# Performance work log

Hardware: AMD Instinct MI355X
Metric: run time of the kernel (lower is better)

Reference implementation:

```python
import jax, jax.numpy as jnp
import numpy as np

HIDDEN_DIM = 64
VOCAB_SIZE = 64
MEMORY_SLOTS = 8
SEQ_LEN = 32
B = 32768


def setup_inputs() -> dict:
    key = jax.random.key(0)
    ks = jax.random.split(key, 11)
    s = 0.1
    return {
        "seqs": jax.random.randint(ks[0], (B, SEQ_LEN), 0, VOCAB_SIZE),
        "query_tok": jax.random.randint(ks[1], (B,), 0, VOCAB_SIZE),
        "embed_table": jax.random.normal(ks[2], (VOCAB_SIZE + 2, HIDDEN_DIM), jnp.float32) * s,
        "sc_w1": jax.random.normal(ks[3], (HIDDEN_DIM, 32), jnp.float32) * s,
        "sc_b1": jax.random.normal(ks[4], (32,), jnp.float32) * s,
        "sc_w2": jax.random.normal(ks[5], (32, 1), jnp.float32) * s,
        "sc_b2": jax.random.normal(ks[6], (1,), jnp.float32) * s,
        "rh_w1": jax.random.normal(ks[7], (2 * HIDDEN_DIM, HIDDEN_DIM), jnp.float32) * s,
        "rh_b1": jax.random.normal(ks[8], (HIDDEN_DIM,), jnp.float32) * s,
        "rh_w2": jax.random.normal(ks[9], (HIDDEN_DIM, VOCAB_SIZE), jnp.float32) * s,
        "rh_b2": jax.random.normal(ks[10], (VOCAB_SIZE,), jnp.float32) * s,
    }


def reference(seqs, query_tok, embed_table, sc_w1, sc_b1, sc_w2, sc_b2,
              rh_w1, rh_b1, rh_w2, rh_b2):
    # Embed the first SEQ_LEN-1 tokens: [B, 31, H]
    embs = embed_table[seqs[:, : SEQ_LEN - 1]]
    slot_ids = jnp.arange(MEMORY_SLOTS)

    def scan_one(embs_b):
        def step(carry, emb):
            mem, count = carry  # mem: [8, H], count: scalar int32
            # score all slots (harmless during fill phase; only used when full)
            scores = (jnp.maximum(mem @ sc_w1 + sc_b1, 0.0) @ sc_w2 + sc_b2)[:, 0]
            evict_idx = jnp.argmin(scores)
            # full: pop evict_idx (shift left above it), append new emb at slot 7
            rolled = jnp.roll(mem, -1, axis=0)
            full_mem = jnp.where(slot_ids[:, None] < evict_idx, mem, rolled)
            full_mem = full_mem.at[MEMORY_SLOTS - 1].set(emb)
            # filling: write new emb at position `count`
            fill_mem = mem.at[jnp.clip(count, 0, MEMORY_SLOTS - 1)].set(emb)
            new_mem = jnp.where(count >= MEMORY_SLOTS, full_mem, fill_mem)
            new_count = jnp.minimum(count + 1, MEMORY_SLOTS)
            return (new_mem, new_count), None

        init = (jnp.zeros((MEMORY_SLOTS, HIDDEN_DIM), embs_b.dtype),
                jnp.array(0, jnp.int32))
        (mem, _), _ = jax.lax.scan(step, init, embs_b)
        return mem.mean(0)  # memory is always full (31 tokens > 8 slots)

    mem_summary = jax.vmap(scan_one)(embs)  # [B, H]
    q_emb = embed_table[query_tok]          # [B, H]
    h = jnp.concatenate([q_emb, mem_summary], axis=-1)  # [B, 2H]
    return jnp.maximum(h @ rh_w1 + rh_b1, 0.0) @ rh_w2 + rh_b2  # [B, VOCAB]
```

## Files before the change

kernel.cpp:

```cpp
#include <hip/hip_runtime.h>


#define SEQ_LEN 32
#define MEM_SLOTS 8

#define WS_SCORE 0
#define WS_Q1B   64
#define WS_M2P   (64 + 4096)
#define WS_W2B   (64 + 4096 + 2048)

typedef __attribute__((ext_vector_type(8)))  short short8;
typedef __attribute__((ext_vector_type(16))) float floatx16;

__device__ __forceinline__ uint32_t bf16rtne(float f) {
    uint32_t u = __float_as_uint(f);
    return (u + 0x7FFFu + ((u >> 16) & 1u)) >> 16;
}

__global__ __launch_bounds__(256) void lem_precompute(
    const float* __restrict__ embed,
    const float* __restrict__ sc_w1, const float* __restrict__ sc_b1,
    const float* __restrict__ sc_w2, const float* __restrict__ sc_b2,
    const float* __restrict__ rh_w1, const float* __restrict__ rh_b1,
    const float* __restrict__ rh_w2,
    float* __restrict__ ws)
{
    const int t = threadIdx.x;
    const int blk = blockIdx.x;
    if (blk < 16) {
        const int p = blk * 256 + t;
        const int v = p >> 6, k = p & 63;
        const float* e = embed + v * 64;
        float q = rh_b1[k];
        #pragma unroll 8
        for (int i = 0; i < 64; ++i) q = fmaf(e[i], rh_w1[i * 64 + k], q);
        ws[WS_Q1B + v * 64 + k] = q;
    } else if (blk < 24) {
        const int p = (blk - 16) * 256 + t;
        const int v = p >> 5, j = p & 31;
        const float* e = embed + v * 64;
        float m0 = 0.f, m1 = 0.f;
        #pragma unroll 8
        for (int i = 0; i < 64; ++i) {
            const float ei = e[i];
            m0 = fmaf(ei, rh_w1[(64 + i) * 64 + 2 * j + 0], m0);
            m1 = fmaf(ei, rh_w1[(64 + i) * 64 + 2 * j + 1], m1);
        }
        ((uint32_t*)ws)[WS_M2P + j * 64 + v] =
            bf16rtne(m0 * 0.125f) | (bf16rtne(m1 * 0.125f) << 16);
    } else {
        __shared__ float part[2048];
        #pragma unroll
        for (int r = 0; r < 8; ++r) {
            const int s = r * 256 + t;
            const int v = s >> 5, k = s & 31;
            const float* e = embed + v * 64;
            float a = sc_b1[k];
            #pragma unroll 8
            for (int i = 0; i < 64; ++i) a = fmaf(e[i], sc_w1[i * 32 + k], a);
            a = fmaxf(a, 0.f);
            part[s] = a * sc_w2[k];
        }
        uint32_t* wb = (uint32_t*)ws + WS_W2B;
        #pragma unroll
        for (int r = 0; r < 8; ++r) {
            const int sidx = r * 256 + t;
            const int d = sidx & 3;
            const int ln = (sidx >> 2) & 63;
            const int tile = sidx >> 8;
            const int ktile = tile >> 1, tn = tile & 1;
            const int k = ktile * 16 + (ln >> 5) * 8 + 2 * d;
            const int n = tn * 32 + (ln & 31);
            wb[sidx] = bf16rtne(rh_w2[k * 64 + n]) |
                       (bf16rtne(rh_w2[(k + 1) * 64 + n]) << 16);
        }
        __syncthreads();
        if (t < 64) {
            float s = sc_b2[0];
            for (int k = 0; k < 32; ++k) s += part[t * 32 + k];
            ws[WS_SCORE + t] = s;
        }
    }
}

__global__ __launch_bounds__(256) void lem_main(
    const int* __restrict__ seqs, const int* __restrict__ qtok,
    const float* __restrict__ rh_b2,
    const float* __restrict__ ws, float* __restrict__ out)
{
    __shared__ uint32_t MT2[2048];
    __shared__ float score_s[64];
    __shared__ unsigned long long tok_s[64];
    __shared__ uint32_t hh2[2048];

    const int t = threadIdx.x;
    const int gbase = blockIdx.x * 64;
    const int lane = t & 63;
    const int w = t >> 6;
    const int col = t & 31;
    const int half = (t >> 5) & 1;
    const int tile_n = w & 1;
    const int tile_m = w >> 1;

    uint4 bq[4];
    const uint4* B4 = (const uint4*)((const uint32_t*)ws + WS_W2B);
    #pragma unroll
    for (int kt = 0; kt < 4; ++kt)
        bq[kt] = B4[(kt * 2 + tile_n) * 64 + lane];
    const float bias = rh_b2[tile_n * 32 + col];
    const int qb = qtok[gbase + lane];
    float4 qreg[4];
    {
        const float4* Q4 = (const float4*)(ws + WS_Q1B);
        const int qbase = (qb * 64 + w * 16) >> 2;
        #pragma unroll
        for (int j4 = 0; j4 < 4; ++j4) qreg[j4] = Q4[qbase + j4];
    }

    if (w == 0) {
        score_s[lane] = ws[WS_SCORE + lane];
        const int b = gbase + lane;
        int tk[SEQ_LEN];
        const int4* sq4 = (const int4*)(seqs + (long long)b * SEQ_LEN);
        #pragma unroll
        for (int r = 0; r < SEQ_LEN / 4; ++r) {
            int4 v = sq4[r];
            tk[r * 4 + 0] = v.x; tk[r * 4 + 1] = v.y;
            tk[r * 4 + 2] = v.z; tk[r * 4 + 3] = v.w;
        }
        int tok[MEM_SLOTS]; float sc[MEM_SLOTS];
        #pragma unroll
        for (int j = 0; j < MEM_SLOTS; ++j) tok[j] = tk[j];
        #pragma unroll
        for (int j = 0; j < MEM_SLOTS; ++j) sc[j] = score_s[tok[j]];
        #pragma unroll
        for (int step = MEM_SLOTS; step < SEQ_LEN - 1; ++step) {
            const int nt = tk[step];
            const float ns = score_s[nt];
            float bv = sc[0]; int be = 0;
            #pragma unroll
            for (int j = 1; j < MEM_SLOTS; ++j) {
                const bool lt = sc[j] < bv;
                bv = lt ? sc[j] : bv;
                be = lt ? j : be;
            }
            #pragma unroll
            for (int j = 0; j < MEM_SLOTS - 1; ++j) {
                const bool take = (j >= be);
                sc[j]  = take ? sc[j + 1]  : sc[j];
                tok[j] = take ? tok[j + 1] : tok[j];
            }
            sc[MEM_SLOTS - 1] = ns;
            tok[MEM_SLOTS - 1] = nt;
        }
        unsigned long long pk = 0ull;
        #pragma unroll
        for (int j = 0; j < MEM_SLOTS; ++j)
            pk |= (unsigned long long)(tok[j] & 255) << (8 * j);
        tok_s[lane] = pk;
    } else {
        const uint4* src = (const uint4*)((const uint32_t*)ws + WS_M2P);
        uint4* dst = (uint4*)MT2;
        for (int i = t - 64; i < 512; i += 192) dst[i] = src[i];
    }
    __syncthreads();

    const int b = lane;
    const unsigned long long pk = tok_s[b];

    float acc[16];
    #pragma unroll
    for (int j4 = 0; j4 < 4; ++j4) {
        acc[j4 * 4 + 0] = qreg[j4].x; acc[j4 * 4 + 1] = qreg[j4].y;
        acc[j4 * 4 + 2] = qreg[j4].z; acc[j4 * 4 + 3] = qreg[j4].w;
    }
    #pragma unroll
    for (int j = 0; j < MEM_SLOTS; ++j) {
        const int tkn = (int)((pk >> (8 * j)) & 255);
        #pragma unroll
        for (int jj = 0; jj < 8; ++jj) {
            const uint32_t u = MT2[(w * 8 + jj) * 64 + tkn];
            acc[2 * jj + 0] += __uint_as_float(u << 16);
            acc[2 * jj + 1] += __uint_as_float(u & 0xFFFF0000u);
        }
    }
    #pragma unroll
    for (int jj = 0; jj < 8; ++jj) {
        const uint32_t lo = (__float_as_uint(fmaxf(acc[2 * jj + 0], 0.f)) + 0x8000u) >> 16;
        const uint32_t hi = (__float_as_uint(fmaxf(acc[2 * jj + 1], 0.f)) + 0x8000u) >> 16;
        hh2[(w * 8 + jj) * 64 + b] = lo | (hi << 16);
    }
    __syncthreads();

    floatx16 oacc;
    #pragma unroll
    for (int i = 0; i < 16; ++i) oacc[i] = bias;

    union U8 { uint32_t u[4]; short8 s; };
    #pragma unroll
    for (int kt = 0; kt < 4; ++kt) {
        U8 a;
        #pragma unroll
        for (int d = 0; d < 4; ++d)
            a.u[d] = hh2[(kt * 8 + half * 4 + d) * 64 + (tile_m * 32 + col)];
        U8 bb;
        bb.u[0] = bq[kt].x; bb.u[1] = bq[kt].y;
        bb.u[2] = bq[kt].z; bb.u[3] = bq[kt].w;
        oacc = __builtin_amdgcn_mfma_f32_32x32x16_bf16(a.s, bb.s, oacc, 0, 0, 0);
    }

    #pragma unroll
    for (int reg = 0; reg < 16; ++reg) {
        const int row = (reg & 3) + 8 * (reg >> 2) + 4 * half;
        out[(long long)(gbase + tile_m * 32 + row) * 64 + tile_n * 32 + col] = oacc[reg];
    }
}

extern "C" void kernel_launch(void* const* d_in, const int* in_sizes, int n_in,
                              void* d_out, int out_size, void* d_ws, size_t ws_size,
                              hipStream_t stream)
{
    const int*   seqs   = (const int*)d_in[0];
    const int*   qtok   = (const int*)d_in[1];
    const float* embed  = (const float*)d_in[2];
    const float* sc_w1  = (const float*)d_in[3];
    const float* sc_b1  = (const float*)d_in[4];
    const float* sc_w2  = (const float*)d_in[5];
    const float* sc_b2  = (const float*)d_in[6];
    const float* rh_w1  = (const float*)d_in[7];
    const float* rh_b1  = (const float*)d_in[8];
    const float* rh_w2  = (const float*)d_in[9];
    const float* rh_b2  = (const float*)d_in[10];
    float* out = (float*)d_out;
    float* ws  = (float*)d_ws;

    const int B = in_sizes[1];

    lem_precompute<<<25, 256, 0, stream>>>(embed, sc_w1, sc_b1, sc_w2, sc_b2,
                                           rh_w1, rh_b1, rh_w2, ws);
    lem_main<<<B / 64, 256, 0, stream>>>(seqs, qtok, rh_b2, ws, out);
}
```

Before: 93.08 us.

## Double block to 512 threads and switch output GEMM to 16x16x32 MFMA tiles

Each block now uses 8 waves instead of 4, so every wave gathers and sums only 8 hidden columns instead of 16. The output GEMM switches from 32x32x16 to 16x16x32 bf16 MFMA, with each wave computing two 16x16 tiles, and the rh_w2 packing in precompute is reordered to match. The hidden buffer in shared memory is padded to a stride of 66 to reduce bank conflicts. The serial eviction scan is still run by one wave per block, so the extra waves mostly sit idle at the barrier.

```diff
diff --git a/kernel.cpp b/kernel.cpp
--- a/kernel.cpp
+++ b/kernel.cpp
@@ -9,8 +9,10 @@
 #define WS_M2P   (64 + 4096)
 #define WS_W2B   (64 + 4096 + 2048)
 
-typedef __attribute__((ext_vector_type(8)))  short short8;
-typedef __attribute__((ext_vector_type(16))) float floatx16;
+#define HH_STRIDE 66
+
+typedef __attribute__((ext_vector_type(8))) short short8;
+typedef __attribute__((ext_vector_type(4))) float floatx4;
 
 __device__ __forceinline__ uint32_t bf16rtne(float f) {
     uint32_t u = __float_as_uint(f);
@@ -67,10 +69,10 @@
             const int sidx = r * 256 + t;
             const int d = sidx & 3;
             const int ln = (sidx >> 2) & 63;
-            const int tile = sidx >> 8;
-            const int ktile = tile >> 1, tn = tile & 1;
-            const int k = ktile * 16 + (ln >> 5) * 8 + 2 * d;
-            const int n = tn * 32 + (ln & 31);
+            const int c = sidx >> 8;
+            const int s = c >> 2, tn = c & 3;
+            const int k = s * 32 + (ln >> 4) * 8 + 2 * d;
+            const int n = tn * 16 + (ln & 15);
             wb[sidx] = bf16rtne(rh_w2[k * 64 + n]) |
                        (bf16rtne(rh_w2[(k + 1) * 64 + n]) << 16);
         }
@@ -83,7 +85,7 @@
     }
 }
 
-__global__ __launch_bounds__(256) void lem_main(
+__global__ __launch_bounds__(512) void lem_main(
     const int* __restrict__ seqs, const int* __restrict__ qtok,
     const float* __restrict__ rh_b2,
     const float* __restrict__ ws, float* __restrict__ out)
@@ -91,37 +93,40 @@
     __shared__ uint32_t MT2[2048];
     __shared__ float score_s[64];
     __shared__ unsigned long long tok_s[64];
-    __shared__ uint32_t hh2[2048];
+    __shared__ uint32_t hh2[32 * HH_STRIDE];
 
     const int t = threadIdx.x;
     const int gbase = blockIdx.x * 64;
     const int lane = t & 63;
     const int w = t >> 6;
-    const int col = t & 31;
-    const int half = (t >> 5) & 1;
-    const int tile_n = w & 1;
-    const int tile_m = w >> 1;
+    const int b = lane;
+    const int tm = w >> 1;
+    const int tn0 = (w & 1) * 2;
+    const int l4 = lane & 15;
+    const int lg = lane >> 4;
 
     uint4 bq[4];
     const uint4* B4 = (const uint4*)((const uint32_t*)ws + WS_W2B);
     #pragma unroll
-    for (int kt = 0; kt < 4; ++kt)
-        bq[kt] = B4[(kt * 2 + tile_n) * 64 + lane];
-    const float bias = rh_b2[tile_n * 32 + col];
-    const int qb = qtok[gbase + lane];
-    float4 qreg[4];
+    for (int s = 0; s < 2; ++s)
+        #pragma unroll
+        for (int j = 0; j < 2; ++j)
+            bq[s * 2 + j] = B4[(s * 4 + tn0 + j) * 64 + lane];
+    const float bias0 = rh_b2[(tn0 + 0) * 16 + l4];
+    const float bias1 = rh_b2[(tn0 + 1) * 16 + l4];
+    const int qb = qtok[gbase + b];
+    float4 qreg[2];
     {
         const float4* Q4 = (const float4*)(ws + WS_Q1B);
-        const int qbase = (qb * 64 + w * 16) >> 2;
-        #pragma unroll
-        for (int j4 = 0; j4 < 4; ++j4) qreg[j4] = Q4[qbase + j4];
+        const int qbase = (qb * 64 + w * 8) >> 2;
+        qreg[0] = Q4[qbase + 0];
+        qreg[1] = Q4[qbase + 1];
     }
 
     if (w == 0) {
         score_s[lane] = ws[WS_SCORE + lane];
-        const int b = gbase + lane;
         int tk[SEQ_LEN];
-        const int4* sq4 = (const int4*)(seqs + (long long)b * SEQ_LEN);
+        const int4* sq4 = (const int4*)(seqs + (long long)(gbase + lane) * SEQ_LEN);
         #pragma unroll
         for (int r = 0; r < SEQ_LEN / 4; ++r) {
             int4 v = sq4[r];
@@ -161,16 +166,14 @@
     } else {
         const uint4* src = (const uint4*)((const uint32_t*)ws + WS_M2P);
         uint4* dst = (uint4*)MT2;
-        for (int i = t - 64; i < 512; i += 192) dst[i] = src[i];
+        for (int i = t - 64; i < 512; i += 448) dst[i] = src[i];
     }
     __syncthreads();
 
-    const int b = lane;
     const unsigned long long pk = tok_s[b];
-
-    float acc[16];
-    #pragma unroll
-    for (int j4 = 0; j4 < 4; ++j4) {
+    float acc[8];
+    #pragma unroll
+    for (int j4 = 0; j4 < 2; ++j4) {
         acc[j4 * 4 + 0] = qreg[j4].x; acc[j4 * 4 + 1] = qreg[j4].y;
         acc[j4 * 4 + 2] = qreg[j4].z; acc[j4 * 4 + 3] = qreg[j4].w;
     }
@@ -178,41 +181,47 @@
     for (int j = 0; j < MEM_SLOTS; ++j) {
         const int tkn = (int)((pk >> (8 * j)) & 255);
         #pragma unroll
-        for (int jj = 0; jj < 8; ++jj) {
-            const uint32_t u = MT2[(w * 8 + jj) * 64 + tkn];
-            acc[2 * jj + 0] += __uint_as_float(u << 16);
-            acc[2 * jj + 1] += __uint_as_float(u & 0xFFFF0000u);
-        }
-    }
-    #pragma unroll
-    for (int jj = 0; jj < 8; ++jj) {
-        const uint32_t lo = (__float_as_uint(fmaxf(acc[2 * jj + 0], 0.f)) + 0x8000u) >> 16;
-        const uint32_t hi = (__float_as_uint(fmaxf(acc[2 * jj + 1], 0.f)) + 0x8000u) >> 16;
-        hh2[(w * 8 + jj) * 64 + b] = lo | (hi << 16);
+        for (int d = 0; d < 4; ++d) {
+            const uint32_t u = MT2[(w * 4 + d) * 64 + tkn];
+            acc[2 * d + 0] += __uint_as_float(u << 16);
+            acc[2 * d + 1] += __uint_as_float(u & 0xFFFF0000u);
+        }
+    }
+    #pragma unroll
+    for (int d = 0; d < 4; ++d) {
+        const uint32_t lo = (__float_as_uint(fmaxf(acc[2 * d + 0], 0.f)) + 0x8000u) >> 16;
+        const uint32_t hi = (__float_as_uint(fmaxf(acc[2 * d + 1], 0.f)) + 0x8000u) >> 16;
+        hh2[(w * 4 + d) * HH_STRIDE + b] = lo | (hi << 16);
     }
     __syncthreads();
 
-    floatx16 oacc;
-    #pragma unroll
-    for (int i = 0; i < 16; ++i) oacc[i] = bias;
-
     union U8 { uint32_t u[4]; short8 s; };
-    #pragma unroll
-    for (int kt = 0; kt < 4; ++kt) {
-        U8 a;
+    U8 a[2];
+    #pragma unroll
+    for (int s = 0; s < 2; ++s)
         #pragma unroll
         for (int d = 0; d < 4; ++d)
-            a.u[d] = hh2[(kt * 8 + half * 4 + d) * 64 + (tile_m * 32 + col)];
-        U8 bb;
-        bb.u[0] = bq[kt].x; bb.u[1] = bq[kt].y;
-        bb.u[2] = bq[kt].z; bb.u[3] = bq[kt].w;
-        oacc = __builtin_amdgcn_mfma_f32_32x32x16_bf16(a.s, bb.s, oacc, 0, 0, 0);
-    }
-
-    #pragma unroll
-    for (int reg = 0; reg < 16; ++reg) {
-        const int row = (reg & 3) + 8 * (reg >> 2) + 4 * half;
-        out[(long long)(gbase + tile_m * 32 + row) * 64 + tile_n * 32 + col] = oacc[reg];
+            a[s].u[d] = hh2[(s * 16 + lg * 4 + d) * HH_STRIDE + tm * 16 + l4];
+
+    floatx4 o0, o1;
+    #pragma unroll
+    for (int i = 0; i < 4; ++i) { o0[i] = bias0; o1[i] = bias1; }
+    #pragma unroll
+    for (int s = 0; s < 2; ++s) {
+        U8 bb0, bb1;
+        bb0.u[0] = bq[s * 2 + 0].x; bb0.u[1] = bq[s * 2 + 0].y;
+        bb0.u[2] = bq[s * 2 + 0].z; bb0.u[3] = bq[s * 2 + 0].w;
+        bb1.u[0] = bq[s * 2 + 1].x; bb1.u[1] = bq[s * 2 + 1].y;
+        bb1.u[2] = bq[s * 2 + 1].z; bb1.u[3] = bq[s * 2 + 1].w;
+        o0 = __builtin_amdgcn_mfma_f32_16x16x32_bf16(a[s].s, bb0.s, o0, 0, 0, 0);
+        o1 = __builtin_amdgcn_mfma_f32_16x16x32_bf16(a[s].s, bb1.s, o1, 0, 0, 0);
+    }
+
+    #pragma unroll
+    for (int reg = 0; reg < 4; ++reg) {
+        const long long row = gbase + tm * 16 + lg * 4 + reg;
+        out[row * 64 + (tn0 + 0) * 16 + l4] = o0[reg];
+        out[row * 64 + (tn0 + 1) * 16 + l4] = o1[reg];
     }
 }
 
@@ -238,5 +247,5 @@
 
     lem_precompute<<<25, 256, 0, stream>>>(embed, sc_w1, sc_b1, sc_w2, sc_b2,
                                            rh_w1, rh_b1, rh_w2, ws);
-    lem_main<<<B / 64, 256, 0, stream>>>(seqs, qtok, rh_b2, ws, out);
-}
+    lem_main<<<B / 64, 512, 0, stream>>>(seqs, qtok, rh_b2, ws, out);
+}
```

Measured after the change: 95.06 us. +2.1%, slower.
